# Kernel optimization log

Hardware: AMD Instinct MI355X
Metric: run time of the kernel (lower is better)

Reference implementation:

```python
import jax, jax.numpy as jnp
import numpy as np

N_HEADS = 32
N_KV_HEADS = 8
HEAD_DIM = 64
ROPE_THETA = 10000.0
NEG_INF = -1e9


def apply_rope(t, offset=0):
    # t: [B, H, L, hd]; half-split (rotate-half) RoPE convention
    B, H, L, hd = t.shape
    pos = jnp.arange(offset, offset + L, dtype=jnp.float32)            # [L]
    inv_freq = 1.0 / (ROPE_THETA ** (jnp.arange(0, hd, 2, dtype=jnp.float32) / hd))  # [hd/2]
    ang = pos[:, None] * inv_freq[None, :]                              # [L, hd/2]
    cos = jnp.cos(ang).astype(t.dtype)
    sin = jnp.sin(ang).astype(t.dtype)
    t1, t2 = jnp.split(t, 2, axis=-1)                                   # each [B,H,L,hd/2]
    return jnp.concatenate([t1 * cos - t2 * sin, t1 * sin + t2 * cos], axis=-1)


def setup_inputs() -> dict:
    key = jax.random.key(0)
    ks = jax.random.split(key, 6)
    B, L, D = 1, 2048, 2048
    x = jax.random.normal(ks[0], (B, L, D), dtype=jnp.float32)
    attn_scale = jnp.ones((1,), dtype=jnp.float32)
    # causal additive mask: 0 on/below diagonal, -1e9 above
    mask = jnp.where(jnp.tril(jnp.ones((L, L), dtype=bool)), 0.0, NEG_INF).astype(jnp.float32)
    s = 0.02
    Wq = jax.random.normal(ks[1], (N_HEADS * HEAD_DIM, D), dtype=jnp.float32) * s
    Wk = jax.random.normal(ks[2], (N_KV_HEADS * HEAD_DIM, D), dtype=jnp.float32) * s
    Wv = jax.random.normal(ks[3], (N_KV_HEADS * HEAD_DIM, D), dtype=jnp.float32) * s
    Wo = jax.random.normal(ks[4], (D, N_HEADS * HEAD_DIM), dtype=jnp.float32) * s
    return {"x": x, "attn_scale": attn_scale, "mask": mask,
            "Wq": Wq, "Wk": Wk, "Wv": Wv, "Wo": Wo}


def reference(x, attn_scale, mask, Wq, Wk, Wv, Wo):
    B, L, D = x.shape
    scale = HEAD_DIM ** -0.5
    # projections (nn.Linear: y = x @ W.T)
    q = (x @ Wq.T).reshape(B, L, N_HEADS, HEAD_DIM).transpose(0, 2, 1, 3)     # [B,H,L,hd]
    k = (x @ Wk.T).reshape(B, L, N_KV_HEADS, HEAD_DIM).transpose(0, 2, 1, 3)  # [B,Hk,L,hd]
    v = (x @ Wv.T).reshape(B, L, N_KV_HEADS, HEAD_DIM).transpose(0, 2, 1, 3)
    q = apply_rope(q)
    k = apply_rope(k)
    q = q * attn_scale  # elementwise attn_scale applied to queries
    # GQA: repeat kv heads
    rep = N_HEADS // N_KV_HEADS
    k = jnp.repeat(k, rep, axis=1)
    v = jnp.repeat(v, rep, axis=1)
    scores = jnp.einsum('bhld,bhmd->bhlm', q, k) * scale + mask
    probs = jax.nn.softmax(scores, axis=-1)
    out = jnp.einsum('bhlm,bhmd->bhld', probs, v)          # [B,H,L,hd]
    out = out.transpose(0, 2, 1, 3).reshape(B, L, N_HEADS * HEAD_DIM)
    return out @ Wo.T
```

## Files before the change

### kernel.cpp

```cpp
#include <hip/hip_runtime.h>
#include <stdint.h>

typedef short bf16x8 __attribute__((ext_vector_type(8)));
typedef float f32x4 __attribute__((ext_vector_type(4)));

__device__ __forceinline__ unsigned short f2bf(float f) {
  uint32_t u = __float_as_uint(f);
  u = (u + 0x7FFFu + ((u >> 16) & 1u)) >> 16;
  return (unsigned short)u;
}
__device__ __forceinline__ float bf2f(unsigned short h) {
  return __uint_as_float(((uint32_t)h) << 16);
}

__device__ __forceinline__ void gload16(const void* g, void* lds) {
  const __attribute__((address_space(1))) char* gp =
      (const __attribute__((address_space(1))) char*)(uintptr_t)g;
  __attribute__((address_space(3))) char* sp =
      (__attribute__((address_space(3))) char*)(uint32_t)(uintptr_t)lds;
  __builtin_amdgcn_global_load_lds(gp, sp, 16, 0, 0);
}

__global__ void k_cvt_all(const float* __restrict__ x, const float* __restrict__ Wq,
                          const float* __restrict__ Wk, const float* __restrict__ Wv,
                          const float* __restrict__ Wo, unsigned short* __restrict__ xb,
                          unsigned short* __restrict__ Wcat, unsigned short* __restrict__ Wob) {
  int b = blockIdx.x;
  const float* src;
  unsigned short* dst;
  int off;
  if (b < 4096)       { src = x;  dst = xb;                  off = b; }
  else if (b < 8192)  { src = Wq; dst = Wcat;                off = b - 4096; }
  else if (b < 9216)  { src = Wk; dst = Wcat + 2048 * 2048;  off = b - 8192; }
  else if (b < 10240) { src = Wv; dst = Wcat + 2560 * 2048;  off = b - 9216; }
  else                { src = Wo; dst = Wob;                  off = b - 10240; }
  int i = off * 256 + threadIdx.x;
  float4 v = ((const float4*)src)[i];
  ushort4 o;
  o.x = f2bf(v.x); o.y = f2bf(v.y); o.z = f2bf(v.z); o.w = f2bf(v.w);
  ((ushort4*)dst)[i] = o;
}

template <int OUTF32>
__global__ __launch_bounds__(256) void k_gemm(const unsigned short* __restrict__ A,
                                              const unsigned short* __restrict__ B,
                                              void* __restrict__ Cout,
                                              int M, int N, int K) {
  __shared__ unsigned short As[128 * 64];
  __shared__ unsigned short Bs[128 * 64];
  const int tid = threadIdx.x;
  const int w = tid >> 6, lane = tid & 63;
  const int g = lane >> 4, cl = lane & 15;
  const int nTn = N >> 7;
  const int per = gridDim.x >> 3;
  const int bid = (blockIdx.x & 7) * per + (blockIdx.x >> 3);
  const int tm = bid / nTn, tn = bid % nTn;
  const int m0 = tm << 7, n0 = tn << 7;
  const int wm = (w >> 1) << 6, wn = (w & 1) << 6;
  f32x4 acc[4][4] = {};
  for (int kt = 0; kt < K; kt += 64) {
    if (kt) __syncthreads();
#pragma unroll
    for (int it = 0; it < 8; ++it) {
      int cc = tid + it * 256;
      int half = cc >> 10;
      int c3 = cc & 1023;
      int row = c3 >> 3, kb = (c3 & 7) << 4;
      const unsigned short* base = half ? (B + (size_t)(n0 + row) * K + kt)
                                        : (A + (size_t)(m0 + row) * K + kt);
      const char* src = (const char*)base + (kb ^ ((row & 7) << 4));
      char* dstl = (char*)(half ? Bs : As) + c3 * 16;
      gload16(src, dstl);
    }
    asm volatile("s_waitcnt vmcnt(0)" ::: "memory");
    __syncthreads();
#pragma unroll
    for (int ks = 0; ks < 2; ++ks) {
      bf16x8 af[4], bfr[4];
#pragma unroll
      for (int i = 0; i < 4; ++i) {
        int row = wm + i * 16 + cl;
        int kb = ((g << 4) + (ks << 6)) ^ ((row & 7) << 4);
        af[i] = *(const bf16x8*)((const char*)As + row * 128 + kb);
      }
#pragma unroll
      for (int j = 0; j < 4; ++j) {
        int row = wn + j * 16 + cl;
        int kb = ((g << 4) + (ks << 6)) ^ ((row & 7) << 4);
        bfr[j] = *(const bf16x8*)((const char*)Bs + row * 128 + kb);
      }
#pragma unroll
      for (int i = 0; i < 4; ++i)
#pragma unroll
        for (int j = 0; j < 4; ++j)
          acc[i][j] = __builtin_amdgcn_mfma_f32_16x16x32_bf16(af[i], bfr[j], acc[i][j], 0, 0, 0);
    }
  }
#pragma unroll
  for (int i = 0; i < 4; ++i)
#pragma unroll
    for (int j = 0; j < 4; ++j)
#pragma unroll
      for (int r = 0; r < 4; ++r) {
        int row = m0 + wm + i * 16 + (g << 2) + r;
        int col = n0 + wn + j * 16 + cl;
        float v = acc[i][j][r];
        if (OUTF32)
          ((float*)Cout)[(size_t)row * N + col] = v;
        else
          ((unsigned short*)Cout)[(size_t)row * N + col] = f2bf(v);
      }
}

__global__ void k_ropevt(unsigned short* __restrict__ qkv, const float* __restrict__ scale_p,
                         unsigned short* __restrict__ vt) {
  __shared__ unsigned short tl[64][80];
  if (blockIdx.x < 2560) {
    int idx = blockIdx.x * 256 + threadIdx.x;
    int l = idx / 320;
    int u = idx - l * 320;
    int h = u >> 3;
    int i4 = (u & 7) << 2;
    int colbase = (h < 32) ? (h << 6) : (2048 + ((h - 32) << 6));
    unsigned short* p = qkv + (size_t)l * 3072 + colbase + i4;
    float sc = (h < 32) ? (scale_p[0] * 0.125f * 1.4426950408889634f) : 1.0f;
    ushort4 a = *(const ushort4*)p;
    ushort4 b = *(const ushort4*)(p + 32);
    unsigned short av[4] = {a.x, a.y, a.z, a.w};
    unsigned short bv[4] = {b.x, b.y, b.z, b.w};
    unsigned short r1[4], r2[4];
#pragma unroll
    for (int j = 0; j < 4; ++j) {
      int i = i4 + j;
      float invf = __expf(-(float)i * 0.2878231366242557f);
      float ang = (float)l * invf;
      float cs = cosf(ang), sn = sinf(ang);
      float x1 = bf2f(av[j]), x2 = bf2f(bv[j]);
      r1[j] = f2bf((x1 * cs - x2 * sn) * sc);
      r2[j] = f2bf((x1 * sn + x2 * cs) * sc);
    }
    ushort4 oa = {r1[0], r1[1], r1[2], r1[3]};
    ushort4 ob = {r2[0], r2[1], r2[2], r2[3]};
    *(ushort4*)p = oa;
    *(ushort4*)(p + 32) = ob;
  } else {
    const int tid = threadIdx.x;
    const int bb = blockIdx.x - 2560;
    const int hk = bb >> 5, lt = bb & 31;
    const int l0 = lt << 6;
#pragma unroll
    for (int it = 0; it < 2; ++it) {
      int cc = tid + it * 256;
      int lr = cc >> 3, d0 = (cc & 7) << 3;
      uint4 v = *(const uint4*)(qkv + (size_t)(l0 + lr) * 3072 + 2560 + hk * 64 + d0);
      *(uint4*)&tl[lr][d0] = v;
    }
    __syncthreads();
#pragma unroll
    for (int it = 0; it < 2; ++it) {
      int cc = tid + it * 256;
      int dr = cc >> 3, le = (cc & 7) << 3;
      unsigned short tmp[8] __attribute__((aligned(16)));
#pragma unroll
      for (int j = 0; j < 8; ++j) tmp[j] = tl[le + j][dr];
      *(uint4*)(vt + (size_t)(hk * 64 + dr) * 2048 + l0 + le) = *(const uint4*)tmp;
    }
  }
}

__global__ __launch_bounds__(256) void k_attn(const unsigned short* __restrict__ qkv,
                                              const unsigned short* __restrict__ vt,
                                              unsigned short* __restrict__ ao) {
  __shared__ unsigned short Ks[2][64 * 64];
  __shared__ unsigned short Vs[3][64 * 64];
  __shared__ unsigned short Ps[4 * 16 * 64];
  const int tid = threadIdx.x;
  const int w = tid >> 6, lane = tid & 63;
  const int g = lane >> 4, cl = lane & 15;
  const int h = blockIdx.x & 31;
  const int qb = 31 - (blockIdx.x >> 5);
  const int q0 = qb << 6;
  const int hk = h >> 2;
  const int qg = q0 + w * 16 + cl;

  const unsigned short* qptr = qkv + (size_t)qg * 3072 + h * 64 + g * 8;
  bf16x8 qf0 = *(const bf16x8*)qptr;
  bf16x8 qf1 = *(const bf16x8*)(qptr + 32);

  float m_run = -3e38f, l_run = 0.0f;
  f32x4 acc[4] = {};

  const unsigned short* kbase = qkv + 2048 + hk * 64;
  const unsigned short* vbase = vt + (size_t)hk * 64 * 2048;
  char* myP = (char*)Ps + w * 2048;

  auto stageK = [&](int ck, int b) {
    const int kv0 = ck << 6;
#pragma unroll
    for (int it = 0; it < 2; ++it) {
      int cc = tid + it * 256;
      int row = cc >> 3, kb = (cc & 7) << 4;
      const char* src = (const char*)(kbase + (size_t)(kv0 + row) * 3072) + (kb ^ ((row & 7) << 4));
      gload16(src, (char*)Ks[b] + cc * 16);
    }
  };
  auto stageV = [&](int ck, int b) {
    const int kv0 = ck << 6;
#pragma unroll
    for (int it = 0; it < 2; ++it) {
      int cc = tid + it * 256;
      int row = cc >> 3, kb = (cc & 7) << 4;
      const char* src = (const char*)(vbase + (size_t)row * 2048 + kv0) + (kb ^ ((row & 7) << 4));
      gload16(src, (char*)Vs[b] + cc * 16);
    }
  };

  stageK(0, 0); stageV(0, 0);
  if (qb >= 1) { stageK(1, 1); stageV(1, 1); }
  asm volatile("s_waitcnt vmcnt(0)" ::: "memory");
  __syncthreads();

  float svP[4][4];
  {
    const char* Kc = (const char*)Ks[0];
    __builtin_amdgcn_s_setprio(1);
#pragma unroll
    for (int t = 0; t < 4; ++t) {
      f32x4 st = {};
#pragma unroll
      for (int ks = 0; ks < 2; ++ks) {
        int row = t * 16 + cl;
        int kb = ((g << 4) + (ks << 6)) ^ ((row & 7) << 4);
        bf16x8 kf = *(const bf16x8*)(Kc + row * 128 + kb);
        st = __builtin_amdgcn_mfma_f32_16x16x32_bf16(kf, ks ? qf1 : qf0, st, 0, 0, 0);
      }
#pragma unroll
      for (int r = 0; r < 4; ++r) svP[t][r] = st[r];
    }
    __builtin_amdgcn_s_setprio(0);
  }
  __syncthreads();

  for (int i = 0; i <= qb; ++i) {
    if (i + 2 <= qb) { stageK(i + 2, (i + 2) & 1); stageV(i + 2, (i + 2) % 3); }

    float svN[4][4];
    if (i < qb) {
      const char* Kc = (const char*)Ks[(i + 1) & 1];
      __builtin_amdgcn_s_setprio(1);
#pragma unroll
      for (int t = 0; t < 4; ++t) {
        f32x4 st = {};
#pragma unroll
        for (int ks = 0; ks < 2; ++ks) {
          int row = t * 16 + cl;
          int kb = ((g << 4) + (ks << 6)) ^ ((row & 7) << 4);
          bf16x8 kf = *(const bf16x8*)(Kc + row * 128 + kb);
          st = __builtin_amdgcn_mfma_f32_16x16x32_bf16(kf, ks ? qf1 : qf0, st, 0, 0, 0);
        }
#pragma unroll
        for (int r = 0; r < 4; ++r) svN[t][r] = st[r];
      }
      __builtin_amdgcn_s_setprio(0);
    }

    if (i == qb) {
      const int kv0 = i << 6;
#pragma unroll
      for (int t = 0; t < 4; ++t)
#pragma unroll
        for (int r = 0; r < 4; ++r) {
          int kvg = kv0 + t * 16 + (g << 2) + r;
          if (kvg > qg) svP[t][r] = -1e9f;
        }
    }
    float pmax = -3e38f;
#pragma unroll
    for (int t = 0; t < 4; ++t)
      pmax = fmaxf(pmax, fmaxf(fmaxf(svP[t][0], svP[t][1]), fmaxf(svP[t][2], svP[t][3])));
    pmax = fmaxf(pmax, __shfl_xor(pmax, 16));
    pmax = fmaxf(pmax, __shfl_xor(pmax, 32));
    if (!__all(pmax - m_run <= 8.0f)) {
      float m_new = fmaxf(m_run, pmax);
      float fac = __builtin_exp2f(m_run - m_new);
      float fr[4];
#pragma unroll
      for (int r = 0; r < 4; ++r) fr[r] = __shfl(fac, (g << 2) + r);
#pragma unroll
      for (int t = 0; t < 4; ++t) {
        acc[t][0] *= fr[0]; acc[t][1] *= fr[1]; acc[t][2] *= fr[2]; acc[t][3] *= fr[3];
      }
      l_run *= fac;
      m_run = m_new;
    }
    float psum = 0.0f;
#pragma unroll
    for (int t = 0; t < 4; ++t) {
      float e0 = __builtin_exp2f(svP[t][0] - m_run);
      float e1 = __builtin_exp2f(svP[t][1] - m_run);
      float e2 = __builtin_exp2f(svP[t][2] - m_run);
      float e3 = __builtin_exp2f(svP[t][3] - m_run);
      psum += (e0 + e1) + (e2 + e3);
      uint32_t d0, d1;
      asm("v_cvt_pk_bf16_f32 %0, %1, %2" : "=v"(d0) : "v"(e0), "v"(e1));
      asm("v_cvt_pk_bf16_f32 %0, %1, %2" : "=v"(d1) : "v"(e2), "v"(e3));
      uint2 dd; dd.x = d0; dd.y = d1;
      int kb = ((t << 5) + (g << 3)) ^ ((cl & 7) << 4);
      *(uint2*)(myP + cl * 128 + kb) = dd;
    }
    psum += __shfl_xor(psum, 16);
    psum += __shfl_xor(psum, 32);
    l_run += psum;

    {
      const char* Vc = (const char*)Vs[i % 3];
      __builtin_amdgcn_s_setprio(1);
#pragma unroll
      for (int ks = 0; ks < 2; ++ks) {
        int kbp = ((g << 4) + (ks << 6)) ^ ((cl & 7) << 4);
        bf16x8 pf = *(const bf16x8*)(myP + cl * 128 + kbp);
#pragma unroll
        for (int t = 0; t < 4; ++t) {
          int row = t * 16 + cl;
          int kbv = ((g << 4) + (ks << 6)) ^ ((row & 7) << 4);
          bf16x8 vf = *(const bf16x8*)(Vc + row * 128 + kbv);
          acc[t] = __builtin_amdgcn_mfma_f32_16x16x32_bf16(pf, vf, acc[t], 0, 0, 0);
        }
      }
      __builtin_amdgcn_s_setprio(0);
    }

    if (i < qb) {
      asm volatile("s_waitcnt vmcnt(0)" ::: "memory");
      __syncthreads();
#pragma unroll
      for (int t = 0; t < 4; ++t)
#pragma unroll
        for (int r = 0; r < 4; ++r) svP[t][r] = svN[t][r];
    }
  }

  float li[4];
#pragma unroll
  for (int r = 0; r < 4; ++r) li[r] = 1.0f / __shfl(l_run, (g << 2) + r);
#pragma unroll
  for (int t = 0; t < 4; ++t)
#pragma unroll
    for (int r = 0; r < 4; ++r) {
      int row = q0 + w * 16 + (g << 2) + r;
      int col = h * 64 + t * 16 + cl;
      ao[(size_t)row * 2048 + col] = f2bf(acc[t][r] * li[r]);
    }
}

extern "C" void kernel_launch(void* const* d_in, const int* in_sizes, int n_in,
                              void* d_out, int out_size, void* d_ws, size_t ws_size,
                              hipStream_t stream) {
  (void)in_sizes; (void)n_in; (void)out_size; (void)ws_size;
  const float* x  = (const float*)d_in[0];
  const float* sc = (const float*)d_in[1];
  const float* Wq = (const float*)d_in[3];
  const float* Wk = (const float*)d_in[4];
  const float* Wv = (const float*)d_in[5];
  const float* Wo = (const float*)d_in[6];
  float* out = (float*)d_out;
  char* ws = (char*)d_ws;
  unsigned short* xb   = (unsigned short*)(ws);
  unsigned short* Wcat = (unsigned short*)(ws + 8388608);
  unsigned short* Wob  = (unsigned short*)(ws + 20971520);
  unsigned short* QKV  = (unsigned short*)(ws + 29360128);
  unsigned short* VT   = (unsigned short*)(ws + 41943040);
  unsigned short* AO   = (unsigned short*)(ws + 44040192);

  k_cvt_all<<<14336, 256, 0, stream>>>(x, Wq, Wk, Wv, Wo, xb, Wcat, Wob);
  k_gemm<0><<<384, 256, 0, stream>>>(xb, Wcat, QKV, 2048, 3072, 2048);
  k_ropevt<<<2816, 256, 0, stream>>>(QKV, sc, VT);
  k_attn<<<1024, 256, 0, stream>>>(QKV, VT, AO);
  k_gemm<1><<<256, 256, 0, stream>>>(AO, Wob, out, 2048, 2048, 2048);
}
```

Baseline: 141.3 us.

## Double-buffer GEMM LDS and rewrite attention with 32x32 MFMA register-resident P

The GEMM kernel gains double-buffered LDS tiles, so the next K tile is loaded while the current one is computed. The attention kernel is restructured around 32x32x16 MFMA with 128-query blocks, each wave owning 32 rows. Probabilities are kept in registers via v_permlane32_swap instead of round-tripping through LDS, and the grid is halved. This removes the P LDS traffic and the one-step S prefetch pipeline, at the cost of larger accumulators, higher register pressure and less overlap of QK^T with softmax.

```diff
diff --git a/kernel.cpp b/kernel.cpp
--- a/kernel.cpp
+++ b/kernel.cpp
@@ -3,6 +3,7 @@
 
 typedef short bf16x8 __attribute__((ext_vector_type(8)));
 typedef float f32x4 __attribute__((ext_vector_type(4)));
+typedef float f32x16 __attribute__((ext_vector_type(16)));
 
 __device__ __forceinline__ unsigned short f2bf(float f) {
   uint32_t u = __float_as_uint(f);
@@ -46,8 +47,8 @@
                                               const unsigned short* __restrict__ B,
                                               void* __restrict__ Cout,
                                               int M, int N, int K) {
-  __shared__ unsigned short As[128 * 64];
-  __shared__ unsigned short Bs[128 * 64];
+  __shared__ unsigned short As[2][128 * 64];
+  __shared__ unsigned short Bs[2][128 * 64];
   const int tid = threadIdx.x;
   const int w = tid >> 6, lane = tid & 63;
   const int g = lane >> 4, cl = lane & 15;
@@ -58,8 +59,8 @@
   const int m0 = tm << 7, n0 = tn << 7;
   const int wm = (w >> 1) << 6, wn = (w & 1) << 6;
   f32x4 acc[4][4] = {};
-  for (int kt = 0; kt < K; kt += 64) {
-    if (kt) __syncthreads();
+
+  auto stage = [&](int kt, int b) {
 #pragma unroll
     for (int it = 0; it < 8; ++it) {
       int cc = tid + it * 256;
@@ -69,11 +70,18 @@
       const unsigned short* base = half ? (B + (size_t)(n0 + row) * K + kt)
                                         : (A + (size_t)(m0 + row) * K + kt);
       const char* src = (const char*)base + (kb ^ ((row & 7) << 4));
-      char* dstl = (char*)(half ? Bs : As) + c3 * 16;
+      char* dstl = (char*)(half ? Bs[b] : As[b]) + c3 * 16;
       gload16(src, dstl);
     }
-    asm volatile("s_waitcnt vmcnt(0)" ::: "memory");
-    __syncthreads();
+  };
+
+  stage(0, 0);
+  asm volatile("s_waitcnt vmcnt(0)" ::: "memory");
+  __syncthreads();
+  int buf = 0;
+
+  for (int kt = 0; kt < K; kt += 64) {
+    if (kt + 64 < K) stage(kt + 64, buf ^ 1);
 #pragma unroll
     for (int ks = 0; ks < 2; ++ks) {
       bf16x8 af[4], bfr[4];
@@ -81,13 +89,13 @@
       for (int i = 0; i < 4; ++i) {
         int row = wm + i * 16 + cl;
         int kb = ((g << 4) + (ks << 6)) ^ ((row & 7) << 4);
-        af[i] = *(const bf16x8*)((const char*)As + row * 128 + kb);
+        af[i] = *(const bf16x8*)((const char*)As[buf] + row * 128 + kb);
       }
 #pragma unroll
       for (int j = 0; j < 4; ++j) {
         int row = wn + j * 16 + cl;
         int kb = ((g << 4) + (ks << 6)) ^ ((row & 7) << 4);
-        bfr[j] = *(const bf16x8*)((const char*)Bs + row * 128 + kb);
+        bfr[j] = *(const bf16x8*)((const char*)Bs[buf] + row * 128 + kb);
       }
 #pragma unroll
       for (int i = 0; i < 4; ++i)
@@ -95,6 +103,9 @@
         for (int j = 0; j < 4; ++j)
           acc[i][j] = __builtin_amdgcn_mfma_f32_16x16x32_bf16(af[i], bfr[j], acc[i][j], 0, 0, 0);
     }
+    asm volatile("s_waitcnt vmcnt(0)" ::: "memory");
+    __syncthreads();
+    buf ^= 1;
   }
 #pragma unroll
   for (int i = 0; i < 4; ++i)
@@ -172,27 +183,28 @@
                                               const unsigned short* __restrict__ vt,
                                               unsigned short* __restrict__ ao) {
   __shared__ unsigned short Ks[2][64 * 64];
-  __shared__ unsigned short Vs[3][64 * 64];
-  __shared__ unsigned short Ps[4 * 16 * 64];
+  __shared__ unsigned short Vs[2][64 * 64];
   const int tid = threadIdx.x;
   const int w = tid >> 6, lane = tid & 63;
-  const int g = lane >> 4, cl = lane & 15;
+  const int ln = lane & 31, hi = lane >> 5;
   const int h = blockIdx.x & 31;
-  const int qb = 31 - (blockIdx.x >> 5);
-  const int q0 = qb << 6;
+  const int qblk = 15 - (blockIdx.x >> 5);
+  const int q0 = qblk << 7;
   const int hk = h >> 2;
-  const int qg = q0 + w * 16 + cl;
-
-  const unsigned short* qptr = qkv + (size_t)qg * 3072 + h * 64 + g * 8;
-  bf16x8 qf0 = *(const bf16x8*)qptr;
-  bf16x8 qf1 = *(const bf16x8*)(qptr + 32);
+  const int qw = q0 + (w << 5);
+  const int qg = qw + ln;
+  const int swz = (ln & 7) << 4;
+
+  bf16x8 qf[4];
+  const unsigned short* qrow = qkv + (size_t)qg * 3072 + h * 64;
+#pragma unroll
+  for (int s = 0; s < 4; ++s) qf[s] = *(const bf16x8*)(qrow + 16 * s + 8 * hi);
 
   float m_run = -3e38f, l_run = 0.0f;
-  f32x4 acc[4] = {};
+  f32x16 acc0 = {}, acc1 = {};
 
   const unsigned short* kbase = qkv + 2048 + hk * 64;
   const unsigned short* vbase = vt + (size_t)hk * 64 * 2048;
-  char* myP = (char*)Ps + w * 2048;
 
   auto stageK = [&](int ck, int b) {
     const int kv0 = ck << 6;
@@ -215,142 +227,109 @@
     }
   };
 
+  const int nt = 2 * qblk + 2;
   stageK(0, 0); stageV(0, 0);
-  if (qb >= 1) { stageK(1, 1); stageV(1, 1); }
   asm volatile("s_waitcnt vmcnt(0)" ::: "memory");
   __syncthreads();
-
-  float svP[4][4];
-  {
-    const char* Kc = (const char*)Ks[0];
+  int buf = 0;
+
+  for (int i = 0; i < nt; ++i) {
+    if (i + 1 < nt) { stageK(i + 1, buf ^ 1); stageV(i + 1, buf ^ 1); }
+    const char* Kc = (const char*)Ks[buf];
+    const char* Vc = (const char*)Vs[buf];
+    const int kv0 = i << 6;
+
+    f32x16 st0 = {}, st1 = {};
     __builtin_amdgcn_s_setprio(1);
 #pragma unroll
-    for (int t = 0; t < 4; ++t) {
-      f32x4 st = {};
-#pragma unroll
-      for (int ks = 0; ks < 2; ++ks) {
-        int row = t * 16 + cl;
-        int kb = ((g << 4) + (ks << 6)) ^ ((row & 7) << 4);
-        bf16x8 kf = *(const bf16x8*)(Kc + row * 128 + kb);
-        st = __builtin_amdgcn_mfma_f32_16x16x32_bf16(kf, ks ? qf1 : qf0, st, 0, 0, 0);
-      }
-#pragma unroll
-      for (int r = 0; r < 4; ++r) svP[t][r] = st[r];
+    for (int s = 0; s < 4; ++s) {
+      int byt = (32 * s + 16 * hi) ^ swz;
+      bf16x8 k0 = *(const bf16x8*)(Kc + ln * 128 + byt);
+      st0 = __builtin_amdgcn_mfma_f32_32x32x16_bf16(k0, qf[s], st0, 0, 0, 0);
+      bf16x8 k1 = *(const bf16x8*)(Kc + (32 + ln) * 128 + byt);
+      st1 = __builtin_amdgcn_mfma_f32_32x32x16_bf16(k1, qf[s], st1, 0, 0, 0);
     }
     __builtin_amdgcn_s_setprio(0);
-  }
-  __syncthreads();
-
-  for (int i = 0; i <= qb; ++i) {
-    if (i + 2 <= qb) { stageK(i + 2, (i + 2) & 1); stageV(i + 2, (i + 2) % 3); }
-
-    float svN[4][4];
-    if (i < qb) {
-      const char* Kc = (const char*)Ks[(i + 1) & 1];
-      __builtin_amdgcn_s_setprio(1);
-#pragma unroll
-      for (int t = 0; t < 4; ++t) {
-        f32x4 st = {};
-#pragma unroll
-        for (int ks = 0; ks < 2; ++ks) {
-          int row = t * 16 + cl;
-          int kb = ((g << 4) + (ks << 6)) ^ ((row & 7) << 4);
-          bf16x8 kf = *(const bf16x8*)(Kc + row * 128 + kb);
-          st = __builtin_amdgcn_mfma_f32_16x16x32_bf16(kf, ks ? qf1 : qf0, st, 0, 0, 0);
-        }
-#pragma unroll
-        for (int r = 0; r < 4; ++r) svN[t][r] = st[r];
-      }
-      __builtin_amdgcn_s_setprio(0);
-    }
-
-    if (i == qb) {
-      const int kv0 = i << 6;
-#pragma unroll
-      for (int t = 0; t < 4; ++t)
-#pragma unroll
-        for (int r = 0; r < 4; ++r) {
-          int kvg = kv0 + t * 16 + (g << 2) + r;
-          if (kvg > qg) svP[t][r] = -1e9f;
-        }
-    }
+
+    if (kv0 + 63 > qw) {
+#pragma unroll
+      for (int r = 0; r < 16; ++r) {
+        int rl = (r & 3) + 8 * (r >> 2) + 4 * hi;
+        if (kv0 + rl > qg) st0[r] = -1e9f;
+        if (kv0 + 32 + rl > qg) st1[r] = -1e9f;
+      }
+    }
+
     float pmax = -3e38f;
 #pragma unroll
-    for (int t = 0; t < 4; ++t)
-      pmax = fmaxf(pmax, fmaxf(fmaxf(svP[t][0], svP[t][1]), fmaxf(svP[t][2], svP[t][3])));
-    pmax = fmaxf(pmax, __shfl_xor(pmax, 16));
+    for (int r = 0; r < 16; ++r) pmax = fmaxf(pmax, fmaxf(st0[r], st1[r]));
     pmax = fmaxf(pmax, __shfl_xor(pmax, 32));
     if (!__all(pmax - m_run <= 8.0f)) {
       float m_new = fmaxf(m_run, pmax);
       float fac = __builtin_exp2f(m_run - m_new);
-      float fr[4];
-#pragma unroll
-      for (int r = 0; r < 4; ++r) fr[r] = __shfl(fac, (g << 2) + r);
-#pragma unroll
-      for (int t = 0; t < 4; ++t) {
-        acc[t][0] *= fr[0]; acc[t][1] *= fr[1]; acc[t][2] *= fr[2]; acc[t][3] *= fr[3];
+#pragma unroll
+      for (int r = 0; r < 16; ++r) {
+        int rl = (r & 3) + 8 * (r >> 2) + 4 * hi;
+        float f = __shfl(fac, rl);
+        acc0[r] *= f; acc1[r] *= f;
       }
       l_run *= fac;
       m_run = m_new;
     }
     float psum = 0.0f;
 #pragma unroll
-    for (int t = 0; t < 4; ++t) {
-      float e0 = __builtin_exp2f(svP[t][0] - m_run);
-      float e1 = __builtin_exp2f(svP[t][1] - m_run);
-      float e2 = __builtin_exp2f(svP[t][2] - m_run);
-      float e3 = __builtin_exp2f(svP[t][3] - m_run);
-      psum += (e0 + e1) + (e2 + e3);
-      uint32_t d0, d1;
-      asm("v_cvt_pk_bf16_f32 %0, %1, %2" : "=v"(d0) : "v"(e0), "v"(e1));
-      asm("v_cvt_pk_bf16_f32 %0, %1, %2" : "=v"(d1) : "v"(e2), "v"(e3));
-      uint2 dd; dd.x = d0; dd.y = d1;
-      int kb = ((t << 5) + (g << 3)) ^ ((cl & 7) << 4);
-      *(uint2*)(myP + cl * 128 + kb) = dd;
-    }
-    psum += __shfl_xor(psum, 16);
+    for (int r = 0; r < 16; ++r) {
+      st0[r] = __builtin_exp2f(st0[r] - m_run);
+      st1[r] = __builtin_exp2f(st1[r] - m_run);
+      psum += st0[r] + st1[r];
+    }
     psum += __shfl_xor(psum, 32);
     l_run += psum;
 
-    {
-      const char* Vc = (const char*)Vs[i % 3];
-      __builtin_amdgcn_s_setprio(1);
-#pragma unroll
-      for (int ks = 0; ks < 2; ++ks) {
-        int kbp = ((g << 4) + (ks << 6)) ^ ((cl & 7) << 4);
-        bf16x8 pf = *(const bf16x8*)(myP + cl * 128 + kbp);
-#pragma unroll
-        for (int t = 0; t < 4; ++t) {
-          int row = t * 16 + cl;
-          int kbv = ((g << 4) + (ks << 6)) ^ ((row & 7) << 4);
-          bf16x8 vf = *(const bf16x8*)(Vc + row * 128 + kbv);
-          acc[t] = __builtin_amdgcn_mfma_f32_16x16x32_bf16(pf, vf, acc[t], 0, 0, 0);
-        }
-      }
-      __builtin_amdgcn_s_setprio(0);
-    }
-
-    if (i < qb) {
-      asm volatile("s_waitcnt vmcnt(0)" ::: "memory");
-      __syncthreads();
-#pragma unroll
-      for (int t = 0; t < 4; ++t)
-#pragma unroll
-        for (int r = 0; r < 4; ++r) svP[t][r] = svN[t][r];
-    }
+    __builtin_amdgcn_s_setprio(1);
+#pragma unroll
+    for (int stile = 0; stile < 2; ++stile) {
+#pragma unroll
+      for (int c = 0; c < 2; ++c) {
+        uint32_t w0, w1, w2, w3;
+        float e0 = (stile ? st1[8 * c + 0] : st0[8 * c + 0]);
+        float e1 = (stile ? st1[8 * c + 1] : st0[8 * c + 1]);
+        float e2 = (stile ? st1[8 * c + 2] : st0[8 * c + 2]);
+        float e3 = (stile ? st1[8 * c + 3] : st0[8 * c + 3]);
+        float e4 = (stile ? st1[8 * c + 4] : st0[8 * c + 4]);
+        float e5 = (stile ? st1[8 * c + 5] : st0[8 * c + 5]);
+        float e6 = (stile ? st1[8 * c + 6] : st0[8 * c + 6]);
+        float e7 = (stile ? st1[8 * c + 7] : st0[8 * c + 7]);
+        asm("v_cvt_pk_bf16_f32 %0, %1, %2" : "=v"(w0) : "v"(e0), "v"(e1));
+        asm("v_cvt_pk_bf16_f32 %0, %1, %2" : "=v"(w2) : "v"(e4), "v"(e5));
+        asm("v_cvt_pk_bf16_f32 %0, %1, %2" : "=v"(w1) : "v"(e2), "v"(e3));
+        asm("v_cvt_pk_bf16_f32 %0, %1, %2" : "=v"(w3) : "v"(e6), "v"(e7));
+        asm("v_permlane32_swap_b32 %0, %1" : "+v"(w0), "+v"(w2));
+        asm("v_permlane32_swap_b32 %0, %1" : "+v"(w1), "+v"(w3));
+        union { uint32_t u[4]; bf16x8 v; } pw;
+        pw.u[0] = w0; pw.u[1] = w1; pw.u[2] = w2; pw.u[3] = w3;
+        int byt = (64 * stile + 32 * c + 16 * hi) ^ swz;
+        bf16x8 v0 = *(const bf16x8*)(Vc + ln * 128 + byt);
+        acc0 = __builtin_amdgcn_mfma_f32_32x32x16_bf16(pw.v, v0, acc0, 0, 0, 0);
+        bf16x8 v1 = *(const bf16x8*)(Vc + (32 + ln) * 128 + byt);
+        acc1 = __builtin_amdgcn_mfma_f32_32x32x16_bf16(pw.v, v1, acc1, 0, 0, 0);
+      }
+    }
+    __builtin_amdgcn_s_setprio(0);
+
+    asm volatile("s_waitcnt vmcnt(0)" ::: "memory");
+    __syncthreads();
+    buf ^= 1;
   }
 
-  float li[4];
-#pragma unroll
-  for (int r = 0; r < 4; ++r) li[r] = 1.0f / __shfl(l_run, (g << 2) + r);
-#pragma unroll
-  for (int t = 0; t < 4; ++t)
-#pragma unroll
-    for (int r = 0; r < 4; ++r) {
-      int row = q0 + w * 16 + (g << 2) + r;
-      int col = h * 64 + t * 16 + cl;
-      ao[(size_t)row * 2048 + col] = f2bf(acc[t][r] * li[r]);
-    }
+#pragma unroll
+  for (int r = 0; r < 16; ++r) {
+    int rl = (r & 3) + 8 * (r >> 2) + 4 * hi;
+    float il = 1.0f / __shfl(l_run, rl);
+    size_t row = (size_t)(qw + rl) * 2048 + h * 64;
+    ao[row + ln] = f2bf(acc0[r] * il);
+    ao[row + 32 + ln] = f2bf(acc1[r] * il);
+  }
 }
 
 extern "C" void kernel_launch(void* const* d_in, const int* in_sizes, int n_in,
@@ -375,6 +354,6 @@
   k_cvt_all<<<14336, 256, 0, stream>>>(x, Wq, Wk, Wv, Wo, xb, Wcat, Wob);
   k_gemm<0><<<384, 256, 0, stream>>>(xb, Wcat, QKV, 2048, 3072, 2048);
   k_ropevt<<<2816, 256, 0, stream>>>(QKV, sc, VT);
-  k_attn<<<1024, 256, 0, stream>>>(QKV, VT, AO);
+  k_attn<<<512, 256, 0, stream>>>(QKV, VT, AO);
   k_gemm<1><<<256, 256, 0, stream>>>(AO, Wob, out, 2048, 2048, 2048);
 }
```

Measured after the change: 139.9 us. Within noise of the previous version (-1.0%).
